# Kernel optimization log

Measured on AMD Instinct MI355X. Metric: run time of the kernel, lower is better.

The kernel has to match this reference:

```python
import jax, jax.numpy as jnp
import numpy as np

N = 100000   # nodes
E = 1600000  # edges (avg degree 16)
D = 128      # in_channels == hidden_channels
H = 4        # heads
C = D // H   # per-head channels = 32


def leaky(x, slope):
    return jnp.where(x >= 0, x, slope * x)


def setup_inputs() -> dict:
    key = jax.random.key(0)
    ks = jax.random.split(key, 12)
    s = 1.0 / np.sqrt(D)
    return {
        "x": jax.random.normal(ks[0], (N, D), jnp.float32),
        "edge_index": jax.random.randint(ks[1], (2, E), 0, N, jnp.int32),
        "edge_type": jax.random.randint(ks[2], (E,), 0, 8, jnp.int32),
        # linear1 (first_layer=True): LeakyReLU(0.01) -> Linear(D, D)
        "W1": jax.random.normal(ks[3], (D, D), jnp.float32) * s,
        "b1": jnp.zeros((D,), jnp.float32),
        # GATConv params: lin (no bias), att_src/att_dst [1,H,C], output bias [H*C]
        "Wg": jax.random.normal(ks[4], (D, D), jnp.float32) * s,
        "att_src": jax.random.normal(ks[5], (1, H, C), jnp.float32) * s,
        "att_dst": jax.random.normal(ks[6], (1, H, C), jnp.float32) * s,
        "bias_g": jnp.zeros((D,), jnp.float32),
        # linear2: LeakyReLU(0.01) -> Linear(D, D)
        "W2": jax.random.normal(ks[7], (D, D), jnp.float32) * s,
        "b2": jnp.zeros((D,), jnp.float32),
    }


def reference(x, edge_index, edge_type, W1, b1, Wg, att_src, att_dst, bias_g, W2, b2):
    # dropout layers act in eval mode (identity); edge_type is unused by forward.
    # linear1: LeakyReLU(0.01) then Linear
    x = leaky(x, 0.01) @ W1.T + b1                      # [N, D]

    # GATConv (add_self_loops=False, concat heads)
    h = (x @ Wg.T).reshape(N, H, C)                     # [N, H, C]
    a_src = jnp.sum(h * att_src, axis=-1)               # [N, H]
    a_dst = jnp.sum(h * att_dst, axis=-1)               # [N, H]

    src, dst = edge_index[0], edge_index[1]
    alpha = leaky(a_src[src] + a_dst[dst], 0.2)          # [E, H]

    # segment softmax over destination nodes (numerically stable)
    amax = jax.ops.segment_max(alpha, dst, num_segments=N)   # [N, H], -inf for empty
    amax = jnp.where(jnp.isfinite(amax), amax, 0.0)
    ex = jnp.exp(alpha - amax[dst])                      # [E, H]
    denom = jax.ops.segment_sum(ex, dst, num_segments=N) # [N, H]
    coeff = ex / (denom[dst] + 1e-16)                    # [E, H]

    msg = h[src] * coeff[:, :, None]                     # [E, H, C]
    out = jax.ops.segment_sum(msg, dst, num_segments=N)  # [N, H, C]
    out = out.reshape(N, H * C) + bias_g                 # [N, D]

    # linear2: LeakyReLU(0.01) then Linear; Dropout(0.3) identity at eval
    out = leaky(out, 0.01) @ W2.T + b2                   # [N, D]
    return out
```

## Files before the change

kernel.cpp:

```cpp
#include <hip/hip_runtime.h>
#include <hip/hip_bf16.h>

#define D128 128

typedef __attribute__((ext_vector_type(8))) short bf16x8;
typedef __attribute__((ext_vector_type(4))) float f32x4;

__device__ __forceinline__ float b2f(unsigned short u) {
    union { unsigned int i; float f; } z;
    z.i = ((unsigned int)u) << 16;
    return z.f;
}

__device__ __forceinline__ unsigned short f2b(float f) {
    union { float f; unsigned int i; } z;
    z.f = f;
    unsigned int r = z.i + 0x7FFFu + ((z.i >> 16) & 1u);
    return (unsigned short)(r >> 16);
}

__device__ __forceinline__ f32x4 mfma16(bf16x8 a, bf16x8 b, f32x4 c) {
    return __builtin_amdgcn_mfma_f32_16x16x32_bf16(a, b, c, 0, 0, 0);
}

#define CHUNK 8192
#define MAXBINS 512
#define BINCAP 8192
#define XBB 1536

__global__ __launch_bounds__(256) void k_prep1(
    const float* __restrict__ x,
    const float* __restrict__ W1, const float* __restrict__ Wg,
    const float* __restrict__ b1,
    const int* __restrict__ ei, int* __restrict__ M,
    float* __restrict__ Wc, float* __restrict__ bc,
    unsigned short* __restrict__ xb,
    int N, int E, int B, int nbins)
{
    __shared__ float wgr[256];
    __shared__ int hist[MAXBINS];
    const int t = threadIdx.x;
    if (blockIdx.x < 64) {
        const int i0 = blockIdx.x * 2;
        wgr[t] = Wg[i0 * 128 + t];
        __syncthreads();
        const int half = t >> 7;
        const int j = t & 127;
        const float* wr = &wgr[half * 128];
        float acc = 0.f;
        #pragma unroll 4
        for (int k = 0; k < 128; ++k)
            acc += wr[k] * W1[k * 128 + j];
        Wc[(i0 + half) * 128 + j] = acc;
        if (j == 0) {
            float ab = 0.f;
            for (int k = 0; k < 128; ++k) ab += wr[k] * b1[k];
            bc[i0 + half] = ab;
        }
    } else if (blockIdx.x < 64 + B) {
        const int chunk = blockIdx.x - 64;
        for (int i = t; i < nbins; i += 256) hist[i] = 0;
        __syncthreads();
        const int base = chunk * CHUNK;
        const int end = min(base + CHUNK, E);
        for (int e = base + t; e < end; e += 256)
            atomicAdd(&hist[ei[E + e] >> 8], 1);
        __syncthreads();
        for (int i = t; i < nbins; i += 256)
            M[i * B + chunk] = hist[i];
    } else {
        const size_t total = (size_t)N * 128;
        const size_t stride = (size_t)XBB * 256 * 8;
        for (size_t i = ((size_t)(blockIdx.x - 64 - B) * 256 + t) * 8; i + 8 <= total; i += stride) {
            float4 f0 = *(const float4*)(x + i);
            float4 f1 = *(const float4*)(x + i + 4);
            float v[8] = { f0.x, f0.y, f0.z, f0.w, f1.x, f1.y, f1.z, f1.w };
            union { uint4 q; unsigned short s[8]; } o;
            #pragma unroll
            for (int jj = 0; jj < 8; ++jj) {
                float f = v[jj];
                f = f >= 0.f ? f : 0.01f * f;
                o.s[jj] = f2b(f);
            }
            *(uint4*)(xb + i) = o.q;
        }
    }
}

__global__ __launch_bounds__(256) void k_prep2(
    const float* __restrict__ Wc, const float* __restrict__ bc,
    const float* __restrict__ att_s, const float* __restrict__ att_d,
    const float* __restrict__ W2,
    unsigned short* __restrict__ Wcat, unsigned short* __restrict__ W2l,
    float* __restrict__ lbias)
{
    const int b = blockIdx.x, t = threadIdx.x;
    if (b < 9) {
        const int q = b * 256 + t;
        const int ct = q >> 8, rem = q & 255;
        const int ks = rem >> 6, lane = rem & 63;
        const int ldiv = lane >> 4, lmod = lane & 15;
        const int kb = ks * 32 + ldiv * 8;
        float v[8];
        if (ct < 8) {
            const int rho = ct * 16 + lmod;
            const float4 a = *(const float4*)(Wc + rho * 128 + kb);
            const float4 bq = *(const float4*)(Wc + rho * 128 + kb + 4);
            v[0] = a.x; v[1] = a.y; v[2] = a.z; v[3] = a.w;
            v[4] = bq.x; v[5] = bq.y; v[6] = bq.z; v[7] = bq.w;
        } else {
            #pragma unroll
            for (int e = 0; e < 8; ++e) v[e] = 0.f;
            if (lmod < 8) {
                const int hh = lmod & 3;
                const float* av = lmod < 4 ? att_s : att_d;
                for (int c = 0; c < 32; ++c) {
                    const float w = av[hh * 32 + c];
                    const float* wrow = Wc + (hh * 32 + c) * 128 + kb;
                    #pragma unroll
                    for (int e = 0; e < 8; ++e) v[e] += w * wrow[e];
                }
            }
        }
        union { uint4 qq; unsigned short s[8]; } o;
        #pragma unroll
        for (int e = 0; e < 8; ++e) o.s[e] = f2b(v[e]);
        *(uint4*)(Wcat + q * 8) = o.qq;
    } else if (b < 17) {
        const int q = (b - 9) * 256 + t;
        const int ct = q >> 8, rem = q & 255;
        const int ks = rem >> 6, lane = rem & 63;
        const int ldiv = lane >> 4, lmod = lane & 15;
        const int kb = ks * 32 + ldiv * 8;
        const int rho = ct * 16 + lmod;
        const float4 a = *(const float4*)(W2 + rho * 128 + kb);
        const float4 bq = *(const float4*)(W2 + rho * 128 + kb + 4);
        union { uint4 qq; unsigned short s[8]; } o;
        o.s[0] = f2b(a.x); o.s[1] = f2b(a.y); o.s[2] = f2b(a.z); o.s[3] = f2b(a.w);
        o.s[4] = f2b(bq.x); o.s[5] = f2b(bq.y); o.s[6] = f2b(bq.z); o.s[7] = f2b(bq.w);
        *(uint4*)(W2l + q * 8) = o.qq;
    } else {
        if (t < 144) {
            float v = 0.f;
            if (t < 128) v = bc[t];
            else if (t < 136) {
                const int hh = (t - 128) & 3;
                const float* av = t < 132 ? att_s : att_d;
                for (int c = 0; c < 32; ++c) v += av[hh * 32 + c] * bc[hh * 32 + c];
            }
            lbias[t] = v;
        }
    }
}

__global__ __launch_bounds__(256) void k_gemm_h(
    const unsigned short* __restrict__ xb,
    const unsigned short* __restrict__ Wcat,
    const float* __restrict__ lbias,
    unsigned short* __restrict__ hfeat,
    float* __restrict__ asrc, float* __restrict__ adst, int N)
{
    __shared__ __align__(16) unsigned short sW[18432];
    const int t = threadIdx.x;
    const int wave = t >> 6, lane = t & 63, lmod = lane & 15, ldiv = lane >> 4;
    const int rowBase = blockIdx.x * 64;

    uint4 w[9];
    #pragma unroll
    for (int r = 0; r < 9; ++r)
        w[r] = *(const uint4*)(Wcat + r * 2048 + t * 8);

    int row = rowBase + wave * 16 + lmod;
    row = min(row, N - 1);
    bf16x8 afr[4];
    #pragma unroll
    for (int ks = 0; ks < 4; ++ks)
        afr[ks] = *(const bf16x8*)(xb + (size_t)row * D128 + ks * 32 + ldiv * 8);

    #pragma unroll
    for (int r = 0; r < 9; ++r)
        *(uint4*)&sW[r * 2048 + t * 8] = w[r];
    __syncthreads();

    f32x4 acc[9] = {};
    #pragma unroll
    for (int ct = 0; ct < 9; ++ct) {
        #pragma unroll
        for (int ks = 0; ks < 4; ++ks) {
            bf16x8 bfr = *(const bf16x8*)&sW[(ct * 256 + ks * 64 + lane) * 8];
            acc[ct] = mfma16(afr[ks], bfr, acc[ct]);
        }
    }

    const int orow = rowBase + wave * 16 + ldiv * 4;
    #pragma unroll
    for (int ct = 0; ct < 8; ++ct) {
        const int col = ct * 16 + lmod;
        const float bias = lbias[col];
        #pragma unroll
        for (int r = 0; r < 4; ++r)
            if (orow + r < N)
                hfeat[(size_t)(orow + r) * D128 + col] = f2b(acc[ct][r] + bias);
    }
    if (lmod < 8) {
        const float lb = lbias[128 + lmod];
        float* dst = lmod < 4 ? asrc : adst;
        const int hh = lmod & 3;
        #pragma unroll
        for (int r = 0; r < 4; ++r)
            if (orow + r < N)
                dst[(size_t)(orow + r) * 4 + hh] = acc[8][r] + lb;
    }
}

__global__ __launch_bounds__(1024) void k_scan1(
    const int* __restrict__ in, int* __restrict__ scanned,
    int* __restrict__ bsum, int n)
{
    __shared__ int lds[1024];
    const int gid = blockIdx.x * 1024 + threadIdx.x;
    const int v = gid < n ? in[gid] : 0;
    lds[threadIdx.x] = v;
    __syncthreads();
    #pragma unroll
    for (int off = 1; off < 1024; off <<= 1) {
        int t = threadIdx.x >= off ? lds[threadIdx.x - off] : 0;
        __syncthreads();
        lds[threadIdx.x] += t;
        __syncthreads();
    }
    if (gid < n) scanned[gid] = lds[threadIdx.x] - v;
    if (threadIdx.x == 1023) bsum[blockIdx.x] = lds[1023];
}

__global__ __launch_bounds__(256) void kA2(
    const int* __restrict__ ei, const int* __restrict__ scanned,
    const int* __restrict__ bsum, int2* __restrict__ binned,
    int E, int B, int nbins, int nM)
{
    __shared__ int cursor[MAXBINS];
    __shared__ int bpre[1024];
    const int nsb = (nM + 1023) >> 10;
    for (int i = threadIdx.x; i < nsb; i += 256) bpre[i] = bsum[i];
    __syncthreads();
    if (threadIdx.x == 0) {
        int run = 0;
        for (int i = 0; i < nsb; ++i) { int tv = bpre[i]; bpre[i] = run; run += tv; }
    }
    __syncthreads();
    for (int i = threadIdx.x; i < nbins; i += 256) {
        const int idx = i * B + blockIdx.x;
        cursor[i] = scanned[idx] + bpre[idx >> 10];
    }
    __syncthreads();
    const int base = blockIdx.x * CHUNK;
    const int end = min(base + CHUNK, E);
    for (int e = base + threadIdx.x; e < end; e += 256) {
        const int s = ei[e], d = ei[E + e];
        const int pos = atomicAdd(&cursor[d >> 8], 1);
        binned[pos] = make_int2(s, d);
    }
}

__global__ __launch_bounds__(256) void kB(
    const int2* __restrict__ binned, const int* __restrict__ scanned,
    const int* __restrict__ bsum, int* __restrict__ bucket,
    int* __restrict__ rowstart, int* __restrict__ rowend,
    int E, int B, int nbins, int N, int nM)
{
    __shared__ int2 eb[BINCAP];
    __shared__ int ldeg[256];
    __shared__ int lscan[256];
    __shared__ int lcur[256];
    __shared__ int bpre[1024];
    const int nsb = (nM + 1023) >> 10;
    for (int i = threadIdx.x; i < nsb; i += 256) bpre[i] = bsum[i];
    __syncthreads();
    if (threadIdx.x == 0) {
        int run = 0;
        for (int i = 0; i < nsb; ++i) { int tv = bpre[i]; bpre[i] = run; run += tv; }
    }
    __syncthreads();
    const int bin = blockIdx.x;
    const int i0 = bin * B;
    const int binstart = scanned[i0] + bpre[i0 >> 10];
    int binend;
    if (bin + 1 < nbins) {
        const int i1 = (bin + 1) * B;
        binend = scanned[i1] + bpre[i1 >> 10];
    } else {
        binend = E;
    }
    int n = binend - binstart;
    if (n > BINCAP) n = BINCAP;

    for (int i = threadIdx.x; i < n; i += 256) eb[i] = binned[binstart + i];
    ldeg[threadIdx.x] = 0;
    __syncthreads();
    for (int i = threadIdx.x; i < n; i += 256)
        atomicAdd(&ldeg[eb[i].y & 255], 1);
    __syncthreads();
    const int v = ldeg[threadIdx.x];
    lscan[threadIdx.x] = v;
    __syncthreads();
    #pragma unroll
    for (int off = 1; off < 256; off <<= 1) {
        int t = threadIdx.x >= off ? lscan[threadIdx.x - off] : 0;
        __syncthreads();
        lscan[threadIdx.x] += t;
        __syncthreads();
    }
    const int excl = lscan[threadIdx.x] - v;
    lcur[threadIdx.x] = excl;
    const int d = (bin << 8) + threadIdx.x;
    if (d < N) {
        rowstart[d] = binstart + excl;
        rowend[d]   = binstart + excl + v;
    }
    __syncthreads();
    for (int i = threadIdx.x; i < n; i += 256) {
        const int lp = atomicAdd(&lcur[eb[i].y & 255], 1);
        bucket[binstart + lp] = eb[i].x;
    }
}

__global__ __launch_bounds__(256) void k_gat(
    const int* __restrict__ bucket,
    const int* __restrict__ rowstart, const int* __restrict__ rowend,
    const float* __restrict__ asrc, const float* __restrict__ adst,
    const unsigned short* __restrict__ hfeat,
    const float* __restrict__ bias_g,
    unsigned short* __restrict__ outbf, int N)
{
    const int wave = threadIdx.x >> 6;
    const int lane = threadIdx.x & 63;
    const int g    = lane >> 4;
    const int gl   = lane & 15;
    const int h    = gl >> 2;
    const int d    = blockIdx.x * 16 + wave * 4 + g;

    int start = 0, end = 0;
    float a_d = 0.f;
    if (d < N) {
        start = rowstart[d];
        end   = rowend[d];
        a_d   = adst[(size_t)d * 4 + h];
    }
    const unsigned int chb = (unsigned int)(gl << 3);
    const unsigned short* hbase = hfeat + chb;

    float acc[8] = {0.f, 0.f, 0.f, 0.f, 0.f, 0.f, 0.f, 0.f};
    float denom = 0.f;

    int j = start;
    for (; j + 4 <= end; j += 4) {
        const int s0 = bucket[j];
        const int s1 = bucket[j + 1];
        const int s2 = bucket[j + 2];
        const int s3 = bucket[j + 3];
        const float as0 = asrc[((size_t)s0 << 2) + h];
        const float as1 = asrc[((size_t)s1 << 2) + h];
        const float as2 = asrc[((size_t)s2 << 2) + h];
        const float as3 = asrc[((size_t)s3 << 2) + h];
        const uint4 hp0 = *(const uint4*)(hbase + ((unsigned int)s0 << 7));
        const uint4 hp1 = *(const uint4*)(hbase + ((unsigned int)s1 << 7));
        const uint4 hp2 = *(const uint4*)(hbase + ((unsigned int)s2 << 7));
        const uint4 hp3 = *(const uint4*)(hbase + ((unsigned int)s3 << 7));
        float a0 = as0 + a_d; a0 = a0 >= 0.f ? a0 : 0.2f * a0;
        float a1 = as1 + a_d; a1 = a1 >= 0.f ? a1 : 0.2f * a1;
        float a2 = as2 + a_d; a2 = a2 >= 0.f ? a2 : 0.2f * a2;
        float a3 = as3 + a_d; a3 = a3 >= 0.f ? a3 : 0.2f * a3;
        const float w0 = __expf(a0), w1 = __expf(a1);
        const float w2 = __expf(a2), w3 = __expf(a3);
        denom += (w0 + w1) + (w2 + w3);
        acc[0] += w0 * b2f((unsigned short)(hp0.x & 0xFFFFu)) + w1 * b2f((unsigned short)(hp1.x & 0xFFFFu))
                + w2 * b2f((unsigned short)(hp2.x & 0xFFFFu)) + w3 * b2f((unsigned short)(hp3.x & 0xFFFFu));
        acc[1] += w0 * b2f((unsigned short)(hp0.x >> 16))     + w1 * b2f((unsigned short)(hp1.x >> 16))
                + w2 * b2f((unsigned short)(hp2.x >> 16))     + w3 * b2f((unsigned short)(hp3.x >> 16));
        acc[2] += w0 * b2f((unsigned short)(hp0.y & 0xFFFFu)) + w1 * b2f((unsigned short)(hp1.y & 0xFFFFu))
                + w2 * b2f((unsigned short)(hp2.y & 0xFFFFu)) + w3 * b2f((unsigned short)(hp3.y & 0xFFFFu));
        acc[3] += w0 * b2f((unsigned short)(hp0.y >> 16))     + w1 * b2f((unsigned short)(hp1.y >> 16))
                + w2 * b2f((unsigned short)(hp2.y >> 16))     + w3 * b2f((unsigned short)(hp3.y >> 16));
        acc[4] += w0 * b2f((unsigned short)(hp0.z & 0xFFFFu)) + w1 * b2f((unsigned short)(hp1.z & 0xFFFFu))
                + w2 * b2f((unsigned short)(hp2.z & 0xFFFFu)) + w3 * b2f((unsigned short)(hp3.z & 0xFFFFu));
        acc[5] += w0 * b2f((unsigned short)(hp0.z >> 16))     + w1 * b2f((unsigned short)(hp1.z >> 16))
                + w2 * b2f((unsigned short)(hp2.z >> 16))     + w3 * b2f((unsigned short)(hp3.z >> 16));
        acc[6] += w0 * b2f((unsigned short)(hp0.w & 0xFFFFu)) + w1 * b2f((unsigned short)(hp1.w & 0xFFFFu))
                + w2 * b2f((unsigned short)(hp2.w & 0xFFFFu)) + w3 * b2f((unsigned short)(hp3.w & 0xFFFFu));
        acc[7] += w0 * b2f((unsigned short)(hp0.w >> 16))     + w1 * b2f((unsigned short)(hp1.w >> 16))
                + w2 * b2f((unsigned short)(hp2.w >> 16))     + w3 * b2f((unsigned short)(hp3.w >> 16));
    }
    for (; j < end; ++j) {
        const int s0 = bucket[j];
        const float as0 = asrc[((size_t)s0 << 2) + h];
        const uint4 hp0 = *(const uint4*)(hbase + ((unsigned int)s0 << 7));
        float a0 = as0 + a_d; a0 = a0 >= 0.f ? a0 : 0.2f * a0;
        const float w0 = __expf(a0);
        denom += w0;
        acc[0] += w0 * b2f((unsigned short)(hp0.x & 0xFFFFu));
        acc[1] += w0 * b2f((unsigned short)(hp0.x >> 16));
        acc[2] += w0 * b2f((unsigned short)(hp0.y & 0xFFFFu));
        acc[3] += w0 * b2f((unsigned short)(hp0.y >> 16));
        acc[4] += w0 * b2f((unsigned short)(hp0.z & 0xFFFFu));
        acc[5] += w0 * b2f((unsigned short)(hp0.z >> 16));
        acc[6] += w0 * b2f((unsigned short)(hp0.w & 0xFFFFu));
        acc[7] += w0 * b2f((unsigned short)(hp0.w >> 16));
    }

    if (d < N) {
        const float inv = 1.f / (denom + 1e-16f);
        const float4 bg0 = *(const float4*)(bias_g + chb);
        const float4 bg1 = *(const float4*)(bias_g + chb + 4);
        const float bg[8] = { bg0.x, bg0.y, bg0.z, bg0.w, bg1.x, bg1.y, bg1.z, bg1.w };
        unsigned short s[8];
        #pragma unroll
        for (int k2 = 0; k2 < 8; ++k2) {
            float v = acc[k2] * inv + bg[k2];
            v = v >= 0.f ? v : 0.01f * v;
            s[k2] = f2b(v);
        }
        uint4 o;
        o.x = ((unsigned int)s[1] << 16) | s[0];
        o.y = ((unsigned int)s[3] << 16) | s[2];
        o.z = ((unsigned int)s[5] << 16) | s[4];
        o.w = ((unsigned int)s[7] << 16) | s[6];
        *(uint4*)(outbf + (((unsigned int)d << 7) + chb)) = o;
    }
}

__global__ __launch_bounds__(256) void k_final(
    const unsigned short* __restrict__ gatbf,
    const unsigned short* __restrict__ W2l,
    const float* __restrict__ b2,
    float* __restrict__ out, int N)
{
    __shared__ __align__(16) unsigned short sW[16384];
    const int t = threadIdx.x;
    const int wave = t >> 6, lane = t & 63, lmod = lane & 15, ldiv = lane >> 4;
    const int rowBase = blockIdx.x * 64;

    uint4 w[8];
    #pragma unroll
    for (int r = 0; r < 8; ++r)
        w[r] = *(const uint4*)(W2l + r * 2048 + t * 8);

    int row = rowBase + wave * 16 + lmod;
    row = min(row, N - 1);
    bf16x8 afr[4];
    #pragma unroll
    for (int ks = 0; ks < 4; ++ks)
        afr[ks] = *(const bf16x8*)(gatbf + (size_t)row * D128 + ks * 32 + ldiv * 8);

    #pragma unroll
    for (int r = 0; r < 8; ++r)
        *(uint4*)&sW[r * 2048 + t * 8] = w[r];
    __syncthreads();

    f32x4 acc[8] = {};
    #pragma unroll
    for (int ct = 0; ct < 8; ++ct) {
        #pragma unroll
        for (int ks = 0; ks < 4; ++ks) {
            bf16x8 bfr = *(const bf16x8*)&sW[(ct * 256 + ks * 64 + lane) * 8];
            acc[ct] = mfma16(afr[ks], bfr, acc[ct]);
        }
    }

    const int orow = rowBase + wave * 16 + ldiv * 4;
    #pragma unroll
    for (int ct = 0; ct < 8; ++ct) {
        const int col = ct * 16 + lmod;
        const float bb = b2[col];
        #pragma unroll
        for (int r = 0; r < 4; ++r)
            if (orow + r < N)
                out[(size_t)(orow + r) * D128 + col] = acc[ct][r] + bb;
    }
}

extern "C" void kernel_launch(void* const* d_in, const int* in_sizes, int n_in,
                              void* d_out, int out_size, void* d_ws, size_t ws_size,
                              hipStream_t stream)
{
    const float* x    = (const float*)d_in[0];
    const int*   ei   = (const int*)d_in[1];
    const float* W1   = (const float*)d_in[3];
    const float* b1   = (const float*)d_in[4];
    const float* Wg   = (const float*)d_in[5];
    const float* atts = (const float*)d_in[6];
    const float* attd = (const float*)d_in[7];
    const float* bg   = (const float*)d_in[8];
    const float* W2   = (const float*)d_in[9];
    const float* b2   = (const float*)d_in[10];
    float* out = (float*)d_out;

    const int N = in_sizes[0] / D128;
    const int E = in_sizes[1] / 2;

    const int B     = (E + CHUNK - 1) / CHUNK;
    const int nbins = (N + 255) >> 8;
    const int nM    = nbins * B;

    char* ws = (char*)d_ws;
    float* Wc = (float*)ws;
    size_t off = 65536;
    float* bc    = (float*)(ws + off); off += 512;
    float* lbias = (float*)(ws + off); off += 1024;
    unsigned short* Wcat = (unsigned short*)(ws + off); off += 36864;
    unsigned short* W2l  = (unsigned short*)(ws + off); off += 32768;
    unsigned short* xb   = (unsigned short*)(ws + off); off += (size_t)N * D128 * 2;
    unsigned short* hfeat = (unsigned short*)(ws + off); off += (size_t)N * D128 * 2;
    float* asrc = (float*)(ws + off); off += (size_t)N * 4 * 4;
    float* adst = (float*)(ws + off); off += (size_t)N * 4 * 4;
    int* M       = (int*)(ws + off); off += (size_t)nM * 4;
    int* scanned = (int*)(ws + off); off += (size_t)nM * 4;
    int* bsum    = (int*)(ws + off); off += 1024 * 4;
    int2* binned = (int2*)(ws + off); off += (size_t)E * 8;
    int* bucket  = (int*)(ws + off); off += (size_t)E * 4;
    int* rowstart = (int*)(ws + off); off += (size_t)N * 4;
    int* rowend   = (int*)(ws + off); off += (size_t)N * 4;
    unsigned short* outbf = (unsigned short*)(ws + off); off += (size_t)N * D128 * 2;

    k_prep1<<<64 + B + XBB, 256, 0, stream>>>(x, W1, Wg, b1, ei, M, Wc, bc, xb,
                                              N, E, B, nbins);
    k_prep2<<<18, 256, 0, stream>>>(Wc, bc, atts, attd, W2, Wcat, W2l, lbias);

    const int nbg = (N + 63) / 64;
    k_gemm_h<<<nbg, 256, 0, stream>>>(xb, Wcat, lbias, hfeat, asrc, adst, N);

    const int nsb = (nM + 1023) / 1024;
    k_scan1<<<nsb, 1024, 0, stream>>>(M, scanned, bsum, nM);
    kA2<<<B, 256, 0, stream>>>(ei, scanned, bsum, binned, E, B, nbins, nM);
    kB<<<nbins, 256, 0, stream>>>(binned, scanned, bsum, bucket,
                                  rowstart, rowend, E, B, nbins, N, nM);

    k_gat<<<(N + 15) / 16, 256, 0, stream>>>(bucket, rowstart, rowend,
                                             asrc, adst, hfeat, bg, outbf, N);

    k_final<<<nbg, 256, 0, stream>>>(outbf, W2l, b2, out, N);
}
```

Measured before the change: 302.6 us.

## Fuse GAT aggregation with final linear and sort bucket sources per row

The final W2 GEMM moves into the GAT aggregation kernel. Each 16-row block stages its bf16 aggregated rows in LDS, and each wave computes two 16-column tiles with MFMA, reading W2 fragments directly from global memory. This removes the intermediate outbf round trip and one kernel launch. Separately, the CSR build packs (dst-low, src) into one word, and each thread insertion-sorts its row's sources so that gathers in the aggregation loop run in ascending address order, at the cost of extra serial work in kB.

```diff
diff --git a/kernel.cpp b/kernel.cpp
--- a/kernel.cpp
+++ b/kernel.cpp
@@ -268,7 +268,8 @@
     int* __restrict__ rowstart, int* __restrict__ rowend,
     int E, int B, int nbins, int N, int nM)
 {
-    __shared__ int2 eb[BINCAP];
+    __shared__ unsigned int pe[BINCAP];
+    __shared__ unsigned int sbuf[BINCAP];
     __shared__ int ldeg[256];
     __shared__ int lscan[256];
     __shared__ int lcur[256];
@@ -294,11 +295,14 @@
     int n = binend - binstart;
     if (n > BINCAP) n = BINCAP;
 
-    for (int i = threadIdx.x; i < n; i += 256) eb[i] = binned[binstart + i];
+    for (int i = threadIdx.x; i < n; i += 256) {
+        const int2 e = binned[binstart + i];
+        pe[i] = ((unsigned int)(e.y & 255) << 20) | (unsigned int)e.x;
+    }
     ldeg[threadIdx.x] = 0;
     __syncthreads();
     for (int i = threadIdx.x; i < n; i += 256)
-        atomicAdd(&ldeg[eb[i].y & 255], 1);
+        atomicAdd(&ldeg[pe[i] >> 20], 1);
     __syncthreads();
     const int v = ldeg[threadIdx.x];
     lscan[threadIdx.x] = v;
@@ -319,10 +323,23 @@
     }
     __syncthreads();
     for (int i = threadIdx.x; i < n; i += 256) {
-        const int lp = atomicAdd(&lcur[eb[i].y & 255], 1);
-        bucket[binstart + lp] = eb[i].x;
-    }
-}
+        const unsigned int p = pe[i];
+        const int lp = atomicAdd(&lcur[p >> 20], 1);
+        sbuf[lp] = p & 0xFFFFFu;
+    }
+    __syncthreads();
+    for (int a = excl + 1; a < excl + v; ++a) {
+        const unsigned int key = sbuf[a];
+        int bp = a - 1;
+        while (bp >= excl && sbuf[bp] > key) { sbuf[bp + 1] = sbuf[bp]; --bp; }
+        sbuf[bp + 1] = key;
+    }
+    __syncthreads();
+    for (int i = threadIdx.x; i < n; i += 256)
+        bucket[binstart + i] = (int)sbuf[i];
+}
+
+#define LDSA 136
 
 __global__ __launch_bounds__(256) void k_gat(
     const int* __restrict__ bucket,
@@ -330,14 +347,18 @@
     const float* __restrict__ asrc, const float* __restrict__ adst,
     const unsigned short* __restrict__ hfeat,
     const float* __restrict__ bias_g,
-    unsigned short* __restrict__ outbf, int N)
-{
+    const unsigned short* __restrict__ W2l,
+    const float* __restrict__ b2,
+    float* __restrict__ out, int N)
+{
+    __shared__ __align__(16) unsigned short sA[16 * LDSA];
     const int wave = threadIdx.x >> 6;
     const int lane = threadIdx.x & 63;
     const int g    = lane >> 4;
     const int gl   = lane & 15;
     const int h    = gl >> 2;
-    const int d    = blockIdx.x * 16 + wave * 4 + g;
+    const int blockBase = blockIdx.x * 16;
+    const int d    = blockBase + wave * 4 + g;
 
     int start = 0, end = 0;
     float a_d = 0.f;
@@ -407,7 +428,7 @@
         acc[7] += w0 * b2f((unsigned short)(hp0.w >> 16));
     }
 
-    if (d < N) {
+    {
         const float inv = 1.f / (denom + 1e-16f);
         const float4 bg0 = *(const float4*)(bias_g + chb);
         const float4 bg1 = *(const float4*)(bias_g + chb + 4);
@@ -424,57 +445,37 @@
         o.y = ((unsigned int)s[3] << 16) | s[2];
         o.z = ((unsigned int)s[5] << 16) | s[4];
         o.w = ((unsigned int)s[7] << 16) | s[6];
-        *(uint4*)(outbf + (((unsigned int)d << 7) + chb)) = o;
-    }
-}
-
-__global__ __launch_bounds__(256) void k_final(
-    const unsigned short* __restrict__ gatbf,
-    const unsigned short* __restrict__ W2l,
-    const float* __restrict__ b2,
-    float* __restrict__ out, int N)
-{
-    __shared__ __align__(16) unsigned short sW[16384];
-    const int t = threadIdx.x;
-    const int wave = t >> 6, lane = t & 63, lmod = lane & 15, ldiv = lane >> 4;
-    const int rowBase = blockIdx.x * 64;
-
-    uint4 w[8];
-    #pragma unroll
-    for (int r = 0; r < 8; ++r)
-        w[r] = *(const uint4*)(W2l + r * 2048 + t * 8);
-
-    int row = rowBase + wave * 16 + lmod;
-    row = min(row, N - 1);
+        *(uint4*)&sA[(wave * 4 + g) * LDSA + (gl << 3)] = o;
+    }
+    __syncthreads();
+
+    const int lmod = lane & 15, ldiv = lane >> 4;
     bf16x8 afr[4];
     #pragma unroll
     for (int ks = 0; ks < 4; ++ks)
-        afr[ks] = *(const bf16x8*)(gatbf + (size_t)row * D128 + ks * 32 + ldiv * 8);
-
-    #pragma unroll
-    for (int r = 0; r < 8; ++r)
-        *(uint4*)&sW[r * 2048 + t * 8] = w[r];
-    __syncthreads();
-
-    f32x4 acc[8] = {};
-    #pragma unroll
-    for (int ct = 0; ct < 8; ++ct) {
+        afr[ks] = *(const bf16x8*)&sA[lmod * LDSA + ks * 32 + ldiv * 8];
+
+    f32x4 acc2[2] = {};
+    #pragma unroll
+    for (int ct2 = 0; ct2 < 2; ++ct2) {
+        const int ct = wave * 2 + ct2;
         #pragma unroll
         for (int ks = 0; ks < 4; ++ks) {
-            bf16x8 bfr = *(const bf16x8*)&sW[(ct * 256 + ks * 64 + lane) * 8];
-            acc[ct] = mfma16(afr[ks], bfr, acc[ct]);
-        }
-    }
-
-    const int orow = rowBase + wave * 16 + ldiv * 4;
-    #pragma unroll
-    for (int ct = 0; ct < 8; ++ct) {
-        const int col = ct * 16 + lmod;
+            bf16x8 bfr = *(const bf16x8*)(W2l + (size_t)((ct * 4 + ks) * 64 + lane) * 8);
+            acc2[ct2] = mfma16(afr[ks], bfr, acc2[ct2]);
+        }
+    }
+
+    #pragma unroll
+    for (int ct2 = 0; ct2 < 2; ++ct2) {
+        const int col = (wave * 2 + ct2) * 16 + lmod;
         const float bb = b2[col];
         #pragma unroll
-        for (int r = 0; r < 4; ++r)
-            if (orow + r < N)
-                out[(size_t)(orow + r) * D128 + col] = acc[ct][r] + bb;
+        for (int r = 0; r < 4; ++r) {
+            const int row16 = ldiv * 4 + r;
+            const int dd = blockBase + row16;
+            if (dd < N) out[(size_t)dd * D128 + col] = acc2[ct2][r] + bb;
+        }
     }
 }
 
@@ -519,7 +520,6 @@
     int* bucket  = (int*)(ws + off); off += (size_t)E * 4;
     int* rowstart = (int*)(ws + off); off += (size_t)N * 4;
     int* rowend   = (int*)(ws + off); off += (size_t)N * 4;
-    unsigned short* outbf = (unsigned short*)(ws + off); off += (size_t)N * D128 * 2;
 
     k_prep1<<<64 + B + XBB, 256, 0, stream>>>(x, W1, Wg, b1, ei, M, Wc, bc, xb,
                                               N, E, B, nbins);
@@ -535,7 +535,6 @@
                                   rowstart, rowend, E, B, nbins, N, nM);
 
     k_gat<<<(N + 15) / 16, 256, 0, stream>>>(bucket, rowstart, rowend,
-                                             asrc, adst, hfeat, bg, outbf, N);
-
-    k_final<<<nbg, 256, 0, stream>>>(outbf, W2l, b2, out, N);
-}
+                                             asrc, adst, hfeat, bg, W2l, b2,
+                                             out, N);
+}
```

New measurement: 336.9 us. 1.11x slower.

## Split GAT aggregation into per-plane passes with precomputed edge weights

Applied to the files above, without the earlier changes.

Stores h in eight 16-channel planes so each aggregation pass gathers from a compact 3.2MB plane that can stay cache-resident, instead of from the full 25.6MB feature matrix. Edge softmax weights and denominators are now computed once in the bucketing kernel and written to a buffer that reuses the dead xb region. The scan is fused into the prep kernel and the edge binning into the h GEMM kernel to cut launches. The cost is extra traffic for writing and rereading the per-edge weights, plus eight passes that each reread the CSR indices.

```diff
diff --git a/kernel.cpp b/kernel.cpp
--- a/kernel.cpp
+++ b/kernel.cpp
@@ -87,13 +87,16 @@
     }
 }
 
-__global__ __launch_bounds__(256) void k_prep2(
+__global__ __launch_bounds__(256) void k_prep2s(
     const float* __restrict__ Wc, const float* __restrict__ bc,
     const float* __restrict__ att_s, const float* __restrict__ att_d,
     const float* __restrict__ W2,
     unsigned short* __restrict__ Wcat, unsigned short* __restrict__ W2l,
-    float* __restrict__ lbias)
-{
+    float* __restrict__ lbias,
+    const int* __restrict__ M, int* __restrict__ scanned,
+    int* __restrict__ bsum, int nM)
+{
+    __shared__ int lds[256];
     const int b = blockIdx.x, t = threadIdx.x;
     if (b < 9) {
         const int q = b * 256 + t;
@@ -139,7 +142,7 @@
         o.s[0] = f2b(a.x); o.s[1] = f2b(a.y); o.s[2] = f2b(a.z); o.s[3] = f2b(a.w);
         o.s[4] = f2b(bq.x); o.s[5] = f2b(bq.y); o.s[6] = f2b(bq.z); o.s[7] = f2b(bq.w);
         *(uint4*)(W2l + q * 8) = o.qq;
-    } else {
+    } else if (b == 17) {
         if (t < 144) {
             float v = 0.f;
             if (t < 128) v = bc[t];
@@ -150,122 +153,133 @@
             }
             lbias[t] = v;
         }
-    }
-}
-
-__global__ __launch_bounds__(256) void k_gemm_h(
+    } else {
+        const int sid = b - 18;
+        const int g0 = sid * 1024 + t * 4;
+        int v0 = g0     < nM ? M[g0]     : 0;
+        int v1 = g0 + 1 < nM ? M[g0 + 1] : 0;
+        int v2 = g0 + 2 < nM ? M[g0 + 2] : 0;
+        int v3 = g0 + 3 < nM ? M[g0 + 3] : 0;
+        const int s = v0 + v1 + v2 + v3;
+        lds[t] = s;
+        __syncthreads();
+        #pragma unroll
+        for (int off = 1; off < 256; off <<= 1) {
+            int tv = t >= off ? lds[t - off] : 0;
+            __syncthreads();
+            lds[t] += tv;
+            __syncthreads();
+        }
+        int run = lds[t] - s;
+        if (g0     < nM) scanned[g0]     = run;
+        run += v0;
+        if (g0 + 1 < nM) scanned[g0 + 1] = run;
+        run += v1;
+        if (g0 + 2 < nM) scanned[g0 + 2] = run;
+        run += v2;
+        if (g0 + 3 < nM) scanned[g0 + 3] = run;
+        if (t == 255) bsum[sid] = lds[255];
+    }
+}
+
+__global__ __launch_bounds__(256) void k_gemmA2(
     const unsigned short* __restrict__ xb,
     const unsigned short* __restrict__ Wcat,
     const float* __restrict__ lbias,
-    unsigned short* __restrict__ hfeat,
-    float* __restrict__ asrc, float* __restrict__ adst, int N)
-{
-    __shared__ __align__(16) unsigned short sW[18432];
-    const int t = threadIdx.x;
-    const int wave = t >> 6, lane = t & 63, lmod = lane & 15, ldiv = lane >> 4;
-    const int rowBase = blockIdx.x * 64;
-
-    uint4 w[9];
-    #pragma unroll
-    for (int r = 0; r < 9; ++r)
-        w[r] = *(const uint4*)(Wcat + r * 2048 + t * 8);
-
-    int row = rowBase + wave * 16 + lmod;
-    row = min(row, N - 1);
-    bf16x8 afr[4];
-    #pragma unroll
-    for (int ks = 0; ks < 4; ++ks)
-        afr[ks] = *(const bf16x8*)(xb + (size_t)row * D128 + ks * 32 + ldiv * 8);
-
-    #pragma unroll
-    for (int r = 0; r < 9; ++r)
-        *(uint4*)&sW[r * 2048 + t * 8] = w[r];
-    __syncthreads();
-
-    f32x4 acc[9] = {};
-    #pragma unroll
-    for (int ct = 0; ct < 9; ++ct) {
-        #pragma unroll
-        for (int ks = 0; ks < 4; ++ks) {
-            bf16x8 bfr = *(const bf16x8*)&sW[(ct * 256 + ks * 64 + lane) * 8];
-            acc[ct] = mfma16(afr[ks], bfr, acc[ct]);
-        }
-    }
-
-    const int orow = rowBase + wave * 16 + ldiv * 4;
-    #pragma unroll
-    for (int ct = 0; ct < 8; ++ct) {
-        const int col = ct * 16 + lmod;
-        const float bias = lbias[col];
-        #pragma unroll
-        for (int r = 0; r < 4; ++r)
-            if (orow + r < N)
-                hfeat[(size_t)(orow + r) * D128 + col] = f2b(acc[ct][r] + bias);
-    }
-    if (lmod < 8) {
-        const float lb = lbias[128 + lmod];
-        float* dst = lmod < 4 ? asrc : adst;
-        const int hh = lmod & 3;
-        #pragma unroll
-        for (int r = 0; r < 4; ++r)
-            if (orow + r < N)
-                dst[(size_t)(orow + r) * 4 + hh] = acc[8][r] + lb;
-    }
-}
-
-__global__ __launch_bounds__(1024) void k_scan1(
-    const int* __restrict__ in, int* __restrict__ scanned,
-    int* __restrict__ bsum, int n)
-{
-    __shared__ int lds[1024];
-    const int gid = blockIdx.x * 1024 + threadIdx.x;
-    const int v = gid < n ? in[gid] : 0;
-    lds[threadIdx.x] = v;
-    __syncthreads();
-    #pragma unroll
-    for (int off = 1; off < 1024; off <<= 1) {
-        int t = threadIdx.x >= off ? lds[threadIdx.x - off] : 0;
-        __syncthreads();
-        lds[threadIdx.x] += t;
-        __syncthreads();
-    }
-    if (gid < n) scanned[gid] = lds[threadIdx.x] - v;
-    if (threadIdx.x == 1023) bsum[blockIdx.x] = lds[1023];
-}
-
-__global__ __launch_bounds__(256) void kA2(
+    unsigned short* __restrict__ hsplit,
+    float* __restrict__ asrc, float* __restrict__ adst,
     const int* __restrict__ ei, const int* __restrict__ scanned,
     const int* __restrict__ bsum, int2* __restrict__ binned,
-    int E, int B, int nbins, int nM)
-{
-    __shared__ int cursor[MAXBINS];
-    __shared__ int bpre[1024];
-    const int nsb = (nM + 1023) >> 10;
-    for (int i = threadIdx.x; i < nsb; i += 256) bpre[i] = bsum[i];
-    __syncthreads();
-    if (threadIdx.x == 0) {
-        int run = 0;
-        for (int i = 0; i < nsb; ++i) { int tv = bpre[i]; bpre[i] = run; run += tv; }
-    }
-    __syncthreads();
-    for (int i = threadIdx.x; i < nbins; i += 256) {
-        const int idx = i * B + blockIdx.x;
-        cursor[i] = scanned[idx] + bpre[idx >> 10];
-    }
-    __syncthreads();
-    const int base = blockIdx.x * CHUNK;
-    const int end = min(base + CHUNK, E);
-    for (int e = base + threadIdx.x; e < end; e += 256) {
-        const int s = ei[e], d = ei[E + e];
-        const int pos = atomicAdd(&cursor[d >> 8], 1);
-        binned[pos] = make_int2(s, d);
+    int N, int E, int B, int nbins, int nM, int nbg)
+{
+    __shared__ __align__(16) unsigned char smem[36864];
+    const int t = threadIdx.x;
+    if (blockIdx.x < nbg) {
+        unsigned short* sW = (unsigned short*)smem;
+        const int wave = t >> 6, lane = t & 63, lmod = lane & 15, ldiv = lane >> 4;
+        const int rowBase = blockIdx.x * 64;
+        const size_t N16 = (size_t)N * 16;
+
+        uint4 w[9];
+        #pragma unroll
+        for (int r = 0; r < 9; ++r)
+            w[r] = *(const uint4*)(Wcat + r * 2048 + t * 8);
+
+        int row = rowBase + wave * 16 + lmod;
+        row = min(row, N - 1);
+        bf16x8 afr[4];
+        #pragma unroll
+        for (int ks = 0; ks < 4; ++ks)
+            afr[ks] = *(const bf16x8*)(xb + (size_t)row * D128 + ks * 32 + ldiv * 8);
+
+        #pragma unroll
+        for (int r = 0; r < 9; ++r)
+            *(uint4*)&sW[r * 2048 + t * 8] = w[r];
+        __syncthreads();
+
+        f32x4 acc[9] = {};
+        #pragma unroll
+        for (int ct = 0; ct < 9; ++ct) {
+            #pragma unroll
+            for (int ks = 0; ks < 4; ++ks) {
+                bf16x8 bfr = *(const bf16x8*)&sW[(ct * 256 + ks * 64 + lane) * 8];
+                acc[ct] = mfma16(afr[ks], bfr, acc[ct]);
+            }
+        }
+
+        const int orow = rowBase + wave * 16 + ldiv * 4;
+        #pragma unroll
+        for (int ct = 0; ct < 8; ++ct) {
+            const float bias = lbias[ct * 16 + lmod];
+            #pragma unroll
+            for (int r = 0; r < 4; ++r)
+                if (orow + r < N)
+                    hsplit[(size_t)ct * N16 + (size_t)(orow + r) * 16 + lmod] =
+                        f2b(acc[ct][r] + bias);
+        }
+        if (lmod < 8) {
+            const float lb = lbias[128 + lmod];
+            float* dst = lmod < 4 ? asrc : adst;
+            const int hh = lmod & 3;
+            #pragma unroll
+            for (int r = 0; r < 4; ++r)
+                if (orow + r < N)
+                    dst[(size_t)(orow + r) * 4 + hh] = acc[8][r] + lb;
+        }
+    } else {
+        int* cursor = (int*)smem;
+        int* bpre   = (int*)(smem + MAXBINS * 4);
+        const int chunk = blockIdx.x - nbg;
+        const int nsb = (nM + 1023) >> 10;
+        for (int i = t; i < nsb; i += 256) bpre[i] = bsum[i];
+        __syncthreads();
+        if (t == 0) {
+            int run = 0;
+            for (int i = 0; i < nsb; ++i) { int tv = bpre[i]; bpre[i] = run; run += tv; }
+        }
+        __syncthreads();
+        for (int i = t; i < nbins; i += 256) {
+            const int idx = i * B + chunk;
+            cursor[i] = scanned[idx] + bpre[idx >> 10];
+        }
+        __syncthreads();
+        const int base = chunk * CHUNK;
+        const int end = min(base + CHUNK, E);
+        for (int e = base + t; e < end; e += 256) {
+            const int s = ei[e], d = ei[E + e];
+            const int pos = atomicAdd(&cursor[d >> 8], 1);
+            binned[pos] = make_int2(s, d);
+        }
     }
 }
 
 __global__ __launch_bounds__(256) void kB(
     const int2* __restrict__ binned, const int* __restrict__ scanned,
-    const int* __restrict__ bsum, int* __restrict__ bucket,
+    const int* __restrict__ bsum,
+    const float* __restrict__ asrc, const float* __restrict__ adst,
+    int* __restrict__ bucket,
     int* __restrict__ rowstart, int* __restrict__ rowend,
+    float* __restrict__ wexp, float* __restrict__ denom,
     int E, int B, int nbins, int N, int nM)
 {
     __shared__ int2 eb[BINCAP];
@@ -305,9 +319,9 @@
     __syncthreads();
     #pragma unroll
     for (int off = 1; off < 256; off <<= 1) {
-        int t = threadIdx.x >= off ? lscan[threadIdx.x - off] : 0;
-        __syncthreads();
-        lscan[threadIdx.x] += t;
+        int tv = threadIdx.x >= off ? lscan[threadIdx.x - off] : 0;
+        __syncthreads();
+        lscan[threadIdx.x] += tv;
         __syncthreads();
     }
     const int excl = lscan[threadIdx.x] - v;
@@ -322,114 +336,111 @@
         const int lp = atomicAdd(&lcur[eb[i].y & 255], 1);
         bucket[binstart + lp] = eb[i].x;
     }
-}
-
-__global__ __launch_bounds__(256) void k_gat(
+    __syncthreads();
+    if (d < N && v > 0) {
+        const float4 adv = *(const float4*)(adst + (size_t)d * 4);
+        const float ad0 = adv.x, ad1 = adv.y, ad2 = adv.z, ad3 = adv.w;
+        float dn0 = 0.f, dn1 = 0.f, dn2 = 0.f, dn3 = 0.f;
+        const int rs = binstart + excl;
+        for (int i = 0; i < v; ++i) {
+            const int s = bucket[rs + i];
+            const float4 as = *(const float4*)(asrc + (size_t)s * 4);
+            float a0 = as.x + ad0; a0 = a0 >= 0.f ? a0 : 0.2f * a0;
+            float a1 = as.y + ad1; a1 = a1 >= 0.f ? a1 : 0.2f * a1;
+            float a2 = as.z + ad2; a2 = a2 >= 0.f ? a2 : 0.2f * a2;
+            float a3 = as.w + ad3; a3 = a3 >= 0.f ? a3 : 0.2f * a3;
+            const float w0 = __expf(a0), w1 = __expf(a1);
+            const float w2 = __expf(a2), w3 = __expf(a3);
+            wexp[rs + i]                   = w0;
+            wexp[(size_t)E + rs + i]       = w1;
+            wexp[(size_t)2 * E + rs + i]   = w2;
+            wexp[(size_t)3 * E + rs + i]   = w3;
+            dn0 += w0; dn1 += w1; dn2 += w2; dn3 += w3;
+        }
+        *(float4*)(denom + (size_t)d * 4) = make_float4(dn0, dn1, dn2, dn3);
+    } else if (d < N) {
+        *(float4*)(denom + (size_t)d * 4) = make_float4(0.f, 0.f, 0.f, 0.f);
+    }
+}
+
+__global__ __launch_bounds__(256) void k_pass(
     const int* __restrict__ bucket,
     const int* __restrict__ rowstart, const int* __restrict__ rowend,
-    const float* __restrict__ asrc, const float* __restrict__ adst,
-    const unsigned short* __restrict__ hfeat,
+    const float* __restrict__ wexp, const float* __restrict__ denom,
+    const unsigned short* __restrict__ hsplit,
     const float* __restrict__ bias_g,
-    unsigned short* __restrict__ outbf, int N)
-{
-    const int wave = threadIdx.x >> 6;
-    const int lane = threadIdx.x & 63;
-    const int g    = lane >> 4;
-    const int gl   = lane & 15;
-    const int h    = gl >> 2;
-    const int d    = blockIdx.x * 16 + wave * 4 + g;
-
-    int start = 0, end = 0;
-    float a_d = 0.f;
-    if (d < N) {
-        start = rowstart[d];
-        end   = rowend[d];
-        a_d   = adst[(size_t)d * 4 + h];
-    }
-    const unsigned int chb = (unsigned int)(gl << 3);
-    const unsigned short* hbase = hfeat + chb;
+    unsigned short* __restrict__ outsplit,
+    int N, int E, int nbd)
+{
+    const int pass = blockIdx.x / nbd;
+    const int bb   = blockIdx.x - pass * nbd;
+    const int head = pass >> 1;
+    const int t = threadIdx.x;
+    const int grp = t >> 1;
+    const int l   = t & 1;
+    const int d = bb * 128 + grp;
+    if (d >= N) return;
+
+    const size_t N16 = (size_t)N * 16;
+    const int start = rowstart[d];
+    const int end   = rowend[d];
+    const float* wp = wexp + (size_t)head * E;
+    const unsigned short* hp = hsplit + (size_t)pass * N16 + (l << 3);
 
     float acc[8] = {0.f, 0.f, 0.f, 0.f, 0.f, 0.f, 0.f, 0.f};
-    float denom = 0.f;
-
     int j = start;
-    for (; j + 4 <= end; j += 4) {
+    for (; j + 2 <= end; j += 2) {
         const int s0 = bucket[j];
         const int s1 = bucket[j + 1];
-        const int s2 = bucket[j + 2];
-        const int s3 = bucket[j + 3];
-        const float as0 = asrc[((size_t)s0 << 2) + h];
-        const float as1 = asrc[((size_t)s1 << 2) + h];
-        const float as2 = asrc[((size_t)s2 << 2) + h];
-        const float as3 = asrc[((size_t)s3 << 2) + h];
-        const uint4 hp0 = *(const uint4*)(hbase + ((unsigned int)s0 << 7));
-        const uint4 hp1 = *(const uint4*)(hbase + ((unsigned int)s1 << 7));
-        const uint4 hp2 = *(const uint4*)(hbase + ((unsigned int)s2 << 7));
-        const uint4 hp3 = *(const uint4*)(hbase + ((unsigned int)s3 << 7));
-        float a0 = as0 + a_d; a0 = a0 >= 0.f ? a0 : 0.2f * a0;
-        float a1 = as1 + a_d; a1 = a1 >= 0.f ? a1 : 0.2f * a1;
-        float a2 = as2 + a_d; a2 = a2 >= 0.f ? a2 : 0.2f * a2;
-        float a3 = as3 + a_d; a3 = a3 >= 0.f ? a3 : 0.2f * a3;
-        const float w0 = __expf(a0), w1 = __expf(a1);
-        const float w2 = __expf(a2), w3 = __expf(a3);
-        denom += (w0 + w1) + (w2 + w3);
-        acc[0] += w0 * b2f((unsigned short)(hp0.x & 0xFFFFu)) + w1 * b2f((unsigned short)(hp1.x & 0xFFFFu))
-                + w2 * b2f((unsigned short)(hp2.x & 0xFFFFu)) + w3 * b2f((unsigned short)(hp3.x & 0xFFFFu));
-        acc[1] += w0 * b2f((unsigned short)(hp0.x >> 16))     + w1 * b2f((unsigned short)(hp1.x >> 16))
-                + w2 * b2f((unsigned short)(hp2.x >> 16))     + w3 * b2f((unsigned short)(hp3.x >> 16));
-        acc[2] += w0 * b2f((unsigned short)(hp0.y & 0xFFFFu)) + w1 * b2f((unsigned short)(hp1.y & 0xFFFFu))
-                + w2 * b2f((unsigned short)(hp2.y & 0xFFFFu)) + w3 * b2f((unsigned short)(hp3.y & 0xFFFFu));
-        acc[3] += w0 * b2f((unsigned short)(hp0.y >> 16))     + w1 * b2f((unsigned short)(hp1.y >> 16))
-                + w2 * b2f((unsigned short)(hp2.y >> 16))     + w3 * b2f((unsigned short)(hp3.y >> 16));
-        acc[4] += w0 * b2f((unsigned short)(hp0.z & 0xFFFFu)) + w1 * b2f((unsigned short)(hp1.z & 0xFFFFu))
-                + w2 * b2f((unsigned short)(hp2.z & 0xFFFFu)) + w3 * b2f((unsigned short)(hp3.z & 0xFFFFu));
-        acc[5] += w0 * b2f((unsigned short)(hp0.z >> 16))     + w1 * b2f((unsigned short)(hp1.z >> 16))
-                + w2 * b2f((unsigned short)(hp2.z >> 16))     + w3 * b2f((unsigned short)(hp3.z >> 16));
-        acc[6] += w0 * b2f((unsigned short)(hp0.w & 0xFFFFu)) + w1 * b2f((unsigned short)(hp1.w & 0xFFFFu))
-                + w2 * b2f((unsigned short)(hp2.w & 0xFFFFu)) + w3 * b2f((unsigned short)(hp3.w & 0xFFFFu));
-        acc[7] += w0 * b2f((unsigned short)(hp0.w >> 16))     + w1 * b2f((unsigned short)(hp1.w >> 16))
-                + w2 * b2f((unsigned short)(hp2.w >> 16))     + w3 * b2f((unsigned short)(hp3.w >> 16));
-    }
-    for (; j < end; ++j) {
+        const float w0 = wp[j];
+        const float w1 = wp[j + 1];
+        const uint4 h0 = *(const uint4*)(hp + ((size_t)s0 << 4));
+        const uint4 h1 = *(const uint4*)(hp + ((size_t)s1 << 4));
+        acc[0] += w0 * b2f((unsigned short)(h0.x & 0xFFFFu)) + w1 * b2f((unsigned short)(h1.x & 0xFFFFu));
+        acc[1] += w0 * b2f((unsigned short)(h0.x >> 16))     + w1 * b2f((unsigned short)(h1.x >> 16));
+        acc[2] += w0 * b2f((unsigned short)(h0.y & 0xFFFFu)) + w1 * b2f((unsigned short)(h1.y & 0xFFFFu));
+        acc[3] += w0 * b2f((unsigned short)(h0.y >> 16))     + w1 * b2f((unsigned short)(h1.y >> 16));
+        acc[4] += w0 * b2f((unsigned short)(h0.z & 0xFFFFu)) + w1 * b2f((unsigned short)(h1.z & 0xFFFFu));
+        acc[5] += w0 * b2f((unsigned short)(h0.z >> 16))     + w1 * b2f((unsigned short)(h1.z >> 16));
+        acc[6] += w0 * b2f((unsigned short)(h0.w & 0xFFFFu)) + w1 * b2f((unsigned short)(h1.w & 0xFFFFu));
+        acc[7] += w0 * b2f((unsigned short)(h0.w >> 16))     + w1 * b2f((unsigned short)(h1.w >> 16));
+    }
+    if (j < end) {
         const int s0 = bucket[j];
-        const float as0 = asrc[((size_t)s0 << 2) + h];
-        const uint4 hp0 = *(const uint4*)(hbase + ((unsigned int)s0 << 7));
-        float a0 = as0 + a_d; a0 = a0 >= 0.f ? a0 : 0.2f * a0;
-        const float w0 = __expf(a0);
-        denom += w0;
-        acc[0] += w0 * b2f((unsigned short)(hp0.x & 0xFFFFu));
-        acc[1] += w0 * b2f((unsigned short)(hp0.x >> 16));
-        acc[2] += w0 * b2f((unsigned short)(hp0.y & 0xFFFFu));
-        acc[3] += w0 * b2f((unsigned short)(hp0.y >> 16));
-        acc[4] += w0 * b2f((unsigned short)(hp0.z & 0xFFFFu));
-        acc[5] += w0 * b2f((unsigned short)(hp0.z >> 16));
-        acc[6] += w0 * b2f((unsigned short)(hp0.w & 0xFFFFu));
-        acc[7] += w0 * b2f((unsigned short)(hp0.w >> 16));
-    }
-
-    if (d < N) {
-        const float inv = 1.f / (denom + 1e-16f);
-        const float4 bg0 = *(const float4*)(bias_g + chb);
-        const float4 bg1 = *(const float4*)(bias_g + chb + 4);
-        const float bg[8] = { bg0.x, bg0.y, bg0.z, bg0.w, bg1.x, bg1.y, bg1.z, bg1.w };
-        unsigned short s[8];
-        #pragma unroll
-        for (int k2 = 0; k2 < 8; ++k2) {
-            float v = acc[k2] * inv + bg[k2];
-            v = v >= 0.f ? v : 0.01f * v;
-            s[k2] = f2b(v);
-        }
-        uint4 o;
-        o.x = ((unsigned int)s[1] << 16) | s[0];
-        o.y = ((unsigned int)s[3] << 16) | s[2];
-        o.z = ((unsigned int)s[5] << 16) | s[4];
-        o.w = ((unsigned int)s[7] << 16) | s[6];
-        *(uint4*)(outbf + (((unsigned int)d << 7) + chb)) = o;
-    }
+        const float w0 = wp[j];
+        const uint4 h0 = *(const uint4*)(hp + ((size_t)s0 << 4));
+        acc[0] += w0 * b2f((unsigned short)(h0.x & 0xFFFFu));
+        acc[1] += w0 * b2f((unsigned short)(h0.x >> 16));
+        acc[2] += w0 * b2f((unsigned short)(h0.y & 0xFFFFu));
+        acc[3] += w0 * b2f((unsigned short)(h0.y >> 16));
+        acc[4] += w0 * b2f((unsigned short)(h0.z & 0xFFFFu));
+        acc[5] += w0 * b2f((unsigned short)(h0.z >> 16));
+        acc[6] += w0 * b2f((unsigned short)(h0.w & 0xFFFFu));
+        acc[7] += w0 * b2f((unsigned short)(h0.w >> 16));
+    }
+
+    const float inv = 1.f / (denom[(size_t)d * 4 + head] + 1e-16f);
+    const int chb = pass * 16 + l * 8;
+    const float4 bg0 = *(const float4*)(bias_g + chb);
+    const float4 bg1 = *(const float4*)(bias_g + chb + 4);
+    const float bg[8] = { bg0.x, bg0.y, bg0.z, bg0.w, bg1.x, bg1.y, bg1.z, bg1.w };
+    unsigned short s8[8];
+    #pragma unroll
+    for (int k = 0; k < 8; ++k) {
+        float vv = acc[k] * inv + bg[k];
+        vv = vv >= 0.f ? vv : 0.01f * vv;
+        s8[k] = f2b(vv);
+    }
+    uint4 o;
+    o.x = ((unsigned int)s8[1] << 16) | s8[0];
+    o.y = ((unsigned int)s8[3] << 16) | s8[2];
+    o.z = ((unsigned int)s8[5] << 16) | s8[4];
+    o.w = ((unsigned int)s8[7] << 16) | s8[6];
+    *(uint4*)(outsplit + (size_t)pass * N16 + (size_t)d * 16 + l * 8) = o;
 }
 
 __global__ __launch_bounds__(256) void k_final(
-    const unsigned short* __restrict__ gatbf,
+    const unsigned short* __restrict__ outsplit,
     const unsigned short* __restrict__ W2l,
     const float* __restrict__ b2,
     float* __restrict__ out, int N)
@@ -438,6 +449,7 @@
     const int t = threadIdx.x;
     const int wave = t >> 6, lane = t & 63, lmod = lane & 15, ldiv = lane >> 4;
     const int rowBase = blockIdx.x * 64;
+    const size_t N16 = (size_t)N * 16;
 
     uint4 w[8];
     #pragma unroll
@@ -448,8 +460,11 @@
     row = min(row, N - 1);
     bf16x8 afr[4];
     #pragma unroll
-    for (int ks = 0; ks < 4; ++ks)
-        afr[ks] = *(const bf16x8*)(gatbf + (size_t)row * D128 + ks * 32 + ldiv * 8);
+    for (int ks = 0; ks < 4; ++ks) {
+        const int plane = 2 * ks + (ldiv >> 1);
+        const int cho = (ldiv & 1) * 8;
+        afr[ks] = *(const bf16x8*)(outsplit + (size_t)plane * N16 + (size_t)row * 16 + cho);
+    }
 
     #pragma unroll
     for (int r = 0; r < 8; ++r)
@@ -500,6 +515,7 @@
     const int B     = (E + CHUNK - 1) / CHUNK;
     const int nbins = (N + 255) >> 8;
     const int nM    = nbins * B;
+    const int nsb   = (nM + 1023) / 1024;
 
     char* ws = (char*)d_ws;
     float* Wc = (float*)ws;
@@ -509,9 +525,11 @@
     unsigned short* Wcat = (unsigned short*)(ws + off); off += 36864;
     unsigned short* W2l  = (unsigned short*)(ws + off); off += 32768;
     unsigned short* xb   = (unsigned short*)(ws + off); off += (size_t)N * D128 * 2;
-    unsigned short* hfeat = (unsigned short*)(ws + off); off += (size_t)N * D128 * 2;
+    float* wexp = (float*)xb;
+    unsigned short* hsplit = (unsigned short*)(ws + off); off += (size_t)N * D128 * 2;
     float* asrc = (float*)(ws + off); off += (size_t)N * 4 * 4;
     float* adst = (float*)(ws + off); off += (size_t)N * 4 * 4;
+    float* denom = (float*)(ws + off); off += (size_t)N * 4 * 4;
     int* M       = (int*)(ws + off); off += (size_t)nM * 4;
     int* scanned = (int*)(ws + off); off += (size_t)nM * 4;
     int* bsum    = (int*)(ws + off); off += 1024 * 4;
@@ -519,23 +537,21 @@
     int* bucket  = (int*)(ws + off); off += (size_t)E * 4;
     int* rowstart = (int*)(ws + off); off += (size_t)N * 4;
     int* rowend   = (int*)(ws + off); off += (size_t)N * 4;
-    unsigned short* outbf = (unsigned short*)(ws + off); off += (size_t)N * D128 * 2;
+    unsigned short* outsplit = (unsigned short*)(ws + off); off += (size_t)N * D128 * 2;
 
     k_prep1<<<64 + B + XBB, 256, 0, stream>>>(x, W1, Wg, b1, ei, M, Wc, bc, xb,
                                               N, E, B, nbins);
-    k_prep2<<<18, 256, 0, stream>>>(Wc, bc, atts, attd, W2, Wcat, W2l, lbias);
-
+    k_prep2s<<<18 + nsb, 256, 0, stream>>>(Wc, bc, atts, attd, W2, Wcat, W2l,
+                                           lbias, M, scanned, bsum, nM);
     const int nbg = (N + 63) / 64;
-    k_gemm_h<<<nbg, 256, 0, stream>>>(xb, Wcat, lbias, hfeat, asrc, adst, N);
-
-    const int nsb = (nM + 1023) / 1024;
-    k_scan1<<<nsb, 1024, 0, stream>>>(M, scanned, bsum, nM);
-    kA2<<<B, 256, 0, stream>>>(ei, scanned, bsum, binned, E, B, nbins, nM);
-    kB<<<nbins, 256, 0, stream>>>(binned, scanned, bsum, bucket,
-                                  rowstart, rowend, E, B, nbins, N, nM);
-
-    k_gat<<<(N + 15) / 16, 256, 0, stream>>>(bucket, rowstart, rowend,
-                                             asrc, adst, hfeat, bg, outbf, N);
-
-    k_final<<<nbg, 256, 0, stream>>>(outbf, W2l, b2, out, N);
-}
+    k_gemmA2<<<nbg + B, 256, 0, stream>>>(xb, Wcat, lbias, hsplit, asrc, adst,
+                                          ei, scanned, bsum, binned,
+                                          N, E, B, nbins, nM, nbg);
+    kB<<<nbins, 256, 0, stream>>>(binned, scanned, bsum, asrc, adst, bucket,
+                                  rowstart, rowend, wexp, denom,
+                                  E, B, nbins, N, nM);
+    const int nbd = (N + 127) / 128;
+    k_pass<<<8 * nbd, 256, 0, stream>>>(bucket, rowstart, rowend, wexp, denom,
+                                        hsplit, bg, outsplit, N, E, nbd);
+    k_final<<<nbg, 256, 0, stream>>>(outsplit, W2l, b2, out, N);
+}
```

After: 554.9 us. 83.4% more time.
